# Kernel tuning notes

Measured on AMD Instinct MI355X. Metric: run time of the kernel, lower is better.

## Reference

```python
import jax, jax.numpy as jnp
import numpy as np

H = 16  # hidden_size
NUM_MLP = 8   # relu, tanh, elu, silu, gelu, none, selu, softplus
NUM_EXPERTS = 12  # 8 MLPs + abs, modulus, sin, cos


def setup_inputs() -> dict:
    key = jax.random.key(0)
    ks = jax.random.split(key, 6)
    B, S, C = 16, 2048, 16
    x = jax.random.normal(ks[0], (B, S, C, 2), dtype=jnp.float32)
    # Stacked per-expert MLP params: Linear(3 -> H) then Linear(H -> 1).
    # (Torch init zeroes the last layer; we use random weights to exercise the math.)
    W1 = jax.random.normal(ks[1], (NUM_MLP, 3, H), dtype=jnp.float32) * (1.0 / np.sqrt(3.0))
    b1 = jax.random.normal(ks[2], (NUM_MLP, H), dtype=jnp.float32) * 0.02
    W2 = jax.random.normal(ks[3], (NUM_MLP, H, 1), dtype=jnp.float32) * (1.0 / np.sqrt(H))
    b2 = jax.random.normal(ks[4], (NUM_MLP, 1), dtype=jnp.float32) * 0.02
    expert_weights = jnp.full((NUM_EXPERTS,), 1.0 / NUM_EXPERTS, dtype=jnp.float32)
    return {"x": x, "W1": W1, "b1": b1, "W2": W2, "b2": b2,
            "expert_weights": expert_weights}


_ACTS = [
    jax.nn.relu,
    jnp.tanh,
    jax.nn.elu,
    jax.nn.silu,
    lambda v: jax.nn.gelu(v, approximate=False),  # torch nn.GELU default = exact
    lambda v: v,                                   # 'none'
    jax.nn.selu,
    jax.nn.softplus,
]


def reference(x, W1, b1, W2, b2, expert_weights):
    # x: (B, S, C, 2) -> output (B, S, C, 1, 1)
    re, im = x[..., 0], x[..., 1]
    amp = jnp.sqrt(re * re + im * im)            # torch.norm over last dim
    feats = jnp.stack([re, im, amp], axis=-1)    # (B,S,C,3)

    outs = []
    for i, act in enumerate(_ACTS):
        h = act(feats @ W1[i] + b1[i])           # (B,S,C,H)
        outs.append(h @ W2[i] + b2[i])           # (B,S,C,1)

    outs.append((jnp.abs(re) + jnp.abs(im))[..., None])  # 'abs'
    outs.append(amp[..., None])                           # 'modulus'
    outs.append(jnp.sin(amp)[..., None])                  # 'sin'
    outs.append(jnp.cos(amp)[..., None])                  # 'cos'

    expert_outputs = jnp.stack(outs, axis=-1)    # (B,S,C,1,12)
    return jnp.sum(expert_outputs * expert_weights, axis=-1, keepdims=True)  # (B,S,C,1,1)
```

## Files before the change

### kernel.cpp

```cpp
#include <hip/hip_runtime.h>

constexpr int BLK = 256;
constexpr int P   = 2;

typedef float v2f __attribute__((ext_vector_type(2)));

__device__ __forceinline__ v2f splat(float s) { return (v2f){s, s}; }
__device__ __forceinline__ v2f pk_fma(v2f a, v2f b, v2f c) {
    return __builtin_elementwise_fma(a, b, c);
}
__device__ __forceinline__ v2f pk_max0(v2f a) {
    return __builtin_elementwise_max(a, (v2f){0.0f, 0.0f});
}
__device__ __forceinline__ v2f pk_min0(v2f a) {
    return __builtin_elementwise_min(a, (v2f){0.0f, 0.0f});
}
__device__ __forceinline__ v2f pk_clamp(v2f a, float lo, float hi) {
    return __builtin_elementwise_min(__builtin_elementwise_max(a, splat(lo)), splat(hi));
}

__device__ __forceinline__ float fast_rcp(float x) { return __builtin_amdgcn_rcpf(x); }

__device__ __forceinline__ float fast_exp2(float x) {
#if __has_builtin(__builtin_amdgcn_exp2f)
    return __builtin_amdgcn_exp2f(x);
#else
    return __expf(x * 0.6931471805599453f);
#endif
}
__device__ __forceinline__ float fast_log2(float x) {
#if __has_builtin(__builtin_amdgcn_logf)
    return __builtin_amdgcn_logf(x);
#else
    return __log2f(x);
#endif
}

#define LOG2E 1.4426950408889634f
#define LN2   0.6931471805599453f

__device__ __forceinline__ v2f pk_exp2(v2f t) { return (v2f){fast_exp2(t.x), fast_exp2(t.y)}; }
__device__ __forceinline__ v2f pk_rcp(v2f t)  { return (v2f){fast_rcp(t.x),  fast_rcp(t.y)};  }
__device__ __forceinline__ v2f pk_rcp_paired(v2f d) {
    float r = fast_rcp(d.x * d.y);
    return (v2f){r * d.y, r * d.x};
}

template<int A> __device__ __forceinline__ v2f act2(v2f z);
template<> __device__ __forceinline__ v2f act2<0>(v2f z) { return pk_max0(z); }
template<> __device__ __forceinline__ v2f act2<1>(v2f z) {
    v2f xc = pk_clamp(z, -4.5f, 4.5f);
    v2f u  = xc * xc;
    v2f n  = pk_fma(pk_fma(u + 378.0f, u, splat(17325.0f)), u, splat(135135.0f)) * xc;
    v2f d  = pk_fma(pk_fma(pk_fma(u, splat(28.0f), splat(3150.0f)), u, splat(62370.0f)),
                    u, splat(135135.0f));
    return n * pk_rcp_paired(d);
}
template<> __device__ __forceinline__ v2f act2<2>(v2f z) {
    v2f em = pk_exp2(z * LOG2E) - 1.0f;
    return pk_max0(z) + pk_min0(em);
}
template<> __device__ __forceinline__ v2f act2<3>(v2f z) {
    v2f e = pk_exp2(z * (-LOG2E));
    return z * pk_rcp(e + 1.0f);
}
template<> __device__ __forceinline__ v2f act2<4>(v2f z) {
    v2f e = pk_exp2(z * (-1.702f * LOG2E));
    return z * pk_rcp(e + 1.0f);
}
template<> __device__ __forceinline__ v2f act2<5>(v2f z) { return z; }
template<> __device__ __forceinline__ v2f act2<6>(v2f z) {
    const float sc   = 1.0507009873554805f;
    const float scal = 1.7580993408473766f;
    v2f e = pk_exp2(z * LOG2E);
    v2f n = pk_fma(splat(scal), e, splat(-scal));
    return pk_fma(pk_max0(z), splat(sc), pk_min0(n));
}
template<> __device__ __forceinline__ v2f act2<7>(v2f z) {
    v2f a = __builtin_elementwise_abs(z) * (-LOG2E);
    v2f d = pk_exp2(a) + 1.0f;
    v2f l = (v2f){fast_log2(d.x), fast_log2(d.y)};
    return pk_fma(splat(LN2), l, pk_max0(z));
}

template<int A>
__device__ __forceinline__ void run_expert(const float* __restrict__ W1,
                                           const float* __restrict__ b1,
                                           const float* __restrict__ W2,
                                           const float* __restrict__ ew,
                                           v2f re, v2f im, v2f am, v2f& acc) {
    v2f accE = (v2f){0.0f, 0.0f};
#pragma unroll
    for (int h = 0; h < 16; ++h) {
        const float wre = W1[A * 48 + h];
        const float wim = W1[A * 48 + 16 + h];
        const float wam = W1[A * 48 + 32 + h];
        const float bb  = b1[A * 16 + h];
        const float w2  = W2[A * 16 + h];
        v2f z = pk_fma(re, splat(wre),
                pk_fma(im, splat(wim),
                pk_fma(am, splat(wam), splat(bb))));
        accE = pk_fma(act2<A>(z), splat(w2), accE);
    }
    acc = pk_fma(accE, splat(ew[A]), acc);
    __builtin_amdgcn_sched_barrier(0);
}

__global__ __launch_bounds__(BLK, 4)
void moe_kernel(const float* __restrict__ x,
                const float* __restrict__ W1,
                const float* __restrict__ b1,
                const float* __restrict__ W2,
                const float* __restrict__ b2,
                const float* __restrict__ ew,
                float* __restrict__ out, int npts) {
    const int pr = blockIdx.x * BLK + threadIdx.x;
    if (pr * P >= npts) return;

    float bconst = 0.0f;
#pragma unroll
    for (int i = 0; i < 8; ++i) bconst = fmaf(ew[i], b2[i], bconst);

    float4 v = reinterpret_cast<const float4*>(x)[pr];
    v2f re = (v2f){v.x, v.z};
    v2f im = (v2f){v.y, v.w};
    v2f r2 = pk_fma(re, re, im * im);
    v2f am = (v2f){__builtin_amdgcn_sqrtf(r2.x), __builtin_amdgcn_sqrtf(r2.y)};

    const float INV2PI = 0.15915494309189535f;
    v2f s = am * INV2PI;
    v2f sn = (v2f){__builtin_amdgcn_sinf(s.x), __builtin_amdgcn_sinf(s.y)};
    v2f cs = (v2f){__builtin_amdgcn_cosf(s.x), __builtin_amdgcn_cosf(s.y)};

    v2f acc = pk_fma(splat(ew[8]),
                     __builtin_elementwise_abs(re) + __builtin_elementwise_abs(im),
                     splat(bconst));
    acc = pk_fma(splat(ew[9]), am, acc);
    acc = pk_fma(splat(ew[10]), sn, acc);
    acc = pk_fma(splat(ew[11]), cs, acc);

    run_expert<0>(W1, b1, W2, ew, re, im, am, acc);
    run_expert<1>(W1, b1, W2, ew, re, im, am, acc);
    run_expert<2>(W1, b1, W2, ew, re, im, am, acc);
    run_expert<3>(W1, b1, W2, ew, re, im, am, acc);
    run_expert<4>(W1, b1, W2, ew, re, im, am, acc);
    run_expert<5>(W1, b1, W2, ew, re, im, am, acc);
    run_expert<6>(W1, b1, W2, ew, re, im, am, acc);
    run_expert<7>(W1, b1, W2, ew, re, im, am, acc);

    reinterpret_cast<float2*>(out)[pr] = make_float2(acc.x, acc.y);
}

extern "C" void kernel_launch(void* const* d_in, const int* in_sizes, int n_in,
                              void* d_out, int out_size, void* d_ws, size_t ws_size,
                              hipStream_t stream) {
    const float* x  = (const float*)d_in[0];
    const float* W1 = (const float*)d_in[1];
    const float* b1 = (const float*)d_in[2];
    const float* W2 = (const float*)d_in[3];
    const float* b2 = (const float*)d_in[4];
    const float* ew = (const float*)d_in[5];
    float* out = (float*)d_out;

    const int npts = in_sizes[0] / 2;
    const int blocks = (npts + BLK * P - 1) / (BLK * P);
    hipLaunchKernelGGL(moe_kernel, dim3(blocks), dim3(BLK), 0, stream,
                       x, W1, b1, W2, b2, ew, out, npts);
}
```

Measured before the change: 20.62 us.

## Split experts across two thread groups per point pair and combine via LDS

Each block now handles 128 point pairs, and two 128-thread groups each evaluate half of the MLP experts for the same points. Partial sums are combined through shared memory after a barrier. This doubles thread-level parallelism and shortens each thread's dependency chain, at the cost of a __syncthreads and an extra LDS round-trip. It also replaces the rational tanh approximation with an exp2/rcp form, switches sin/cos to __sinf/__cosf, and raises the launch-bounds occupancy hint.

```diff
diff --git a/kernel.cpp b/kernel.cpp
--- a/kernel.cpp
+++ b/kernel.cpp
@@ -1,7 +1,7 @@
 #include <hip/hip_runtime.h>
 
-constexpr int BLK = 256;
-constexpr int P   = 2;
+constexpr int BLK   = 256;
+constexpr int SLOTS = 128;
 
 typedef float v2f __attribute__((ext_vector_type(2)));
 
@@ -14,9 +14,6 @@
 }
 __device__ __forceinline__ v2f pk_min0(v2f a) {
     return __builtin_elementwise_min(a, (v2f){0.0f, 0.0f});
-}
-__device__ __forceinline__ v2f pk_clamp(v2f a, float lo, float hi) {
-    return __builtin_elementwise_min(__builtin_elementwise_max(a, splat(lo)), splat(hi));
 }
 
 __device__ __forceinline__ float fast_rcp(float x) { return __builtin_amdgcn_rcpf(x); }
@@ -41,20 +38,13 @@
 
 __device__ __forceinline__ v2f pk_exp2(v2f t) { return (v2f){fast_exp2(t.x), fast_exp2(t.y)}; }
 __device__ __forceinline__ v2f pk_rcp(v2f t)  { return (v2f){fast_rcp(t.x),  fast_rcp(t.y)};  }
-__device__ __forceinline__ v2f pk_rcp_paired(v2f d) {
-    float r = fast_rcp(d.x * d.y);
-    return (v2f){r * d.y, r * d.x};
-}
 
 template<int A> __device__ __forceinline__ v2f act2(v2f z);
 template<> __device__ __forceinline__ v2f act2<0>(v2f z) { return pk_max0(z); }
 template<> __device__ __forceinline__ v2f act2<1>(v2f z) {
-    v2f xc = pk_clamp(z, -4.5f, 4.5f);
-    v2f u  = xc * xc;
-    v2f n  = pk_fma(pk_fma(u + 378.0f, u, splat(17325.0f)), u, splat(135135.0f)) * xc;
-    v2f d  = pk_fma(pk_fma(pk_fma(u, splat(28.0f), splat(3150.0f)), u, splat(62370.0f)),
-                    u, splat(135135.0f));
-    return n * pk_rcp_paired(d);
+    v2f e = pk_exp2(z * (2.0f * LOG2E));
+    v2f r = pk_rcp(e + 1.0f);
+    return pk_fma(splat(-2.0f), r, splat(1.0f));
 }
 template<> __device__ __forceinline__ v2f act2<2>(v2f z) {
     v2f em = pk_exp2(z * LOG2E) - 1.0f;
@@ -106,7 +96,7 @@
     __builtin_amdgcn_sched_barrier(0);
 }
 
-__global__ __launch_bounds__(BLK, 4)
+__global__ __launch_bounds__(BLK, 8)
 void moe_kernel(const float* __restrict__ x,
                 const float* __restrict__ W1,
                 const float* __restrict__ b1,
@@ -114,41 +104,55 @@
                 const float* __restrict__ b2,
                 const float* __restrict__ ew,
                 float* __restrict__ out, int npts) {
-    const int pr = blockIdx.x * BLK + threadIdx.x;
-    if (pr * P >= npts) return;
+    __shared__ v2f s_part[SLOTS];
 
-    float bconst = 0.0f;
-#pragma unroll
-    for (int i = 0; i < 8; ++i) bconst = fmaf(ew[i], b2[i], bconst);
+    const int slot = threadIdx.x & (SLOTS - 1);
+    const int grp  = threadIdx.x >> 7;
+    const int pr   = blockIdx.x * SLOTS + slot;
+    const bool ok  = (pr * 2 < npts);
 
-    float4 v = reinterpret_cast<const float4*>(x)[pr];
+    float4 v = ok ? reinterpret_cast<const float4*>(x)[pr]
+                  : make_float4(0.0f, 0.0f, 0.0f, 0.0f);
     v2f re = (v2f){v.x, v.z};
     v2f im = (v2f){v.y, v.w};
     v2f r2 = pk_fma(re, re, im * im);
     v2f am = (v2f){__builtin_amdgcn_sqrtf(r2.x), __builtin_amdgcn_sqrtf(r2.y)};
 
-    const float INV2PI = 0.15915494309189535f;
-    v2f s = am * INV2PI;
-    v2f sn = (v2f){__builtin_amdgcn_sinf(s.x), __builtin_amdgcn_sinf(s.y)};
-    v2f cs = (v2f){__builtin_amdgcn_cosf(s.x), __builtin_amdgcn_cosf(s.y)};
+    v2f acc = (v2f){0.0f, 0.0f};
 
-    v2f acc = pk_fma(splat(ew[8]),
+    if (grp == 1) {
+        run_expert<4>(W1, b1, W2, ew, re, im, am, acc);
+        run_expert<5>(W1, b1, W2, ew, re, im, am, acc);
+        run_expert<6>(W1, b1, W2, ew, re, im, am, acc);
+        run_expert<7>(W1, b1, W2, ew, re, im, am, acc);
+        s_part[slot] = acc;
+    } else {
+        float bconst = 0.0f;
+#pragma unroll
+        for (int i = 0; i < 8; ++i) bconst = fmaf(ew[i], b2[i], bconst);
+
+        v2f sn = (v2f){__sinf(am.x), __sinf(am.y)};
+        v2f cs = (v2f){__cosf(am.x), __cosf(am.y)};
+
+        acc = pk_fma(splat(ew[8]),
                      __builtin_elementwise_abs(re) + __builtin_elementwise_abs(im),
                      splat(bconst));
-    acc = pk_fma(splat(ew[9]), am, acc);
-    acc = pk_fma(splat(ew[10]), sn, acc);
-    acc = pk_fma(splat(ew[11]), cs, acc);
+        acc = pk_fma(splat(ew[9]), am, acc);
+        acc = pk_fma(splat(ew[10]), sn, acc);
+        acc = pk_fma(splat(ew[11]), cs, acc);
 
-    run_expert<0>(W1, b1, W2, ew, re, im, am, acc);
-    run_expert<1>(W1, b1, W2, ew, re, im, am, acc);
-    run_expert<2>(W1, b1, W2, ew, re, im, am, acc);
-    run_expert<3>(W1, b1, W2, ew, re, im, am, acc);
-    run_expert<4>(W1, b1, W2, ew, re, im, am, acc);
-    run_expert<5>(W1, b1, W2, ew, re, im, am, acc);
-    run_expert<6>(W1, b1, W2, ew, re, im, am, acc);
-    run_expert<7>(W1, b1, W2, ew, re, im, am, acc);
+        run_expert<0>(W1, b1, W2, ew, re, im, am, acc);
+        run_expert<1>(W1, b1, W2, ew, re, im, am, acc);
+        run_expert<2>(W1, b1, W2, ew, re, im, am, acc);
+        run_expert<3>(W1, b1, W2, ew, re, im, am, acc);
+    }
 
-    reinterpret_cast<float2*>(out)[pr] = make_float2(acc.x, acc.y);
+    __syncthreads();
+
+    if (grp == 0 && ok) {
+        v2f tot = acc + s_part[slot];
+        reinterpret_cast<float2*>(out)[pr] = make_float2(tot.x, tot.y);
+    }
 }
 
 extern "C" void kernel_launch(void* const* d_in, const int* in_sizes, int n_in,
@@ -162,8 +166,9 @@
     const float* ew = (const float*)d_in[5];
     float* out = (float*)d_out;
 
-    const int npts = in_sizes[0] / 2;
-    const int blocks = (npts + BLK * P - 1) / (BLK * P);
+    const int npts  = in_sizes[0] / 2;
+    const int pairs = (npts + 1) / 2;
+    const int blocks = (pairs + SLOTS - 1) / SLOTS;
     hipLaunchKernelGGL(moe_kernel, dim3(blocks), dim3(BLK), 0, stream,
                        x, W1, b1, W2, b2, ew, out, npts);
 }
```

After: 20.29 us. No clear change (-1.6%).
